# Optimization experiments

Hardware: AMD Instinct MI355X
Metric: run time of the kernel (lower is better)

Reference implementation:

```python
import jax, jax.numpy as jnp
import numpy as np

N = 100000
E = 1600000
D_IN = 128
D_OUT = 128
BN_EPS = 1e-5


def setup_inputs() -> dict:
    key = jax.random.key(0)
    k_x, k_src, k_dst, k_val, k_w = jax.random.split(key, 5)
    x = jax.random.normal(k_x, (N, D_IN), dtype=jnp.float32)
    edge_src = jax.random.randint(k_src, (E,), 0, N, dtype=jnp.int64)
    edge_dst = jax.random.randint(k_dst, (E,), 0, N, dtype=jnp.int64)
    edge_vals = jax.random.uniform(k_val, (E,), dtype=jnp.float32)
    # kaiming-uniform-like init for weight
    bound = float(np.sqrt(6.0 / D_IN))
    weight = jax.random.uniform(k_w, (D_IN, D_OUT), dtype=jnp.float32,
                                minval=-bound, maxval=bound)
    bias = jnp.zeros((D_OUT,), dtype=jnp.float32)
    gamma = jnp.ones((D_OUT,), dtype=jnp.float32)   # BatchNorm weight
    beta = jnp.zeros((D_OUT,), dtype=jnp.float32)   # BatchNorm bias
    return {"x": x, "edge_src": edge_src, "edge_dst": edge_dst,
            "edge_vals": edge_vals, "weight": weight, "bias": bias,
            "gamma": gamma, "beta": beta}


def reference(x, edge_src, edge_dst, edge_vals, weight, bias, gamma, beta):
    # SpMM: out[dst] += val * x[src]  (adj @ x with adj in COO form)
    msgs = x[edge_src] * edge_vals[:, None]            # [E, D_IN]
    agg = jax.ops.segment_sum(msgs, edge_dst, num_segments=N)  # [N, D_IN]
    # Dense linear
    h = jnp.dot(agg, weight) + bias                     # [N, D_OUT]
    # BatchNorm1d (training mode: batch statistics, biased variance)
    mean = jnp.mean(h, axis=0)
    var = jnp.mean(jnp.square(h - mean), axis=0)
    h_norm = (h - mean) * jax.lax.rsqrt(var + BN_EPS)
    return h_norm * gamma + beta
```

## Files before the change

kernel.cpp:

```cpp
#include <hip/hip_runtime.h>
#include <math.h>

#define D 128
#define BSHIFT 9
#define BROWS 512
#define TILE 8192
constexpr float BN_EPS = 1e-5f;
typedef unsigned long long ull;

__device__ __forceinline__ unsigned f2bf_rne(float f) {
    unsigned u = __float_as_uint(f);
    return (u + 0x7FFFu + ((u >> 16) & 1u)) >> 16;
}
__device__ __forceinline__ float bf_lo(unsigned u) { return __uint_as_float(u << 16); }
__device__ __forceinline__ float bf_hi(unsigned u) { return __uint_as_float(u & 0xFFFF0000u); }

__global__ __launch_bounds__(256) void phase1_kernel(
    const float* __restrict__ A,
    const float* __restrict__ W,
    unsigned* __restrict__ yb,
    int n,
    const int* __restrict__ esrc, const int* __restrict__ edst,
    const float* __restrict__ evals,
    uint2* __restrict__ slices,
    int* __restrict__ ofs_t,
    int B, int nwgA, int E)
{
    __shared__ __align__(16) char smem[81920];
    const int tid = threadIdx.x;

    if ((int)blockIdx.x < nwgA) {
        int* h   = (int*)smem;
        int* ps  = h + 256;
        int* cur = ps + 256;
        const int wg = blockIdx.x;
        const int e0 = wg * TILE;
        const int e1 = min(e0 + TILE, E);

        h[tid] = 0;
        __syncthreads();
        for (int e = e0 + tid; e < e1; e += 256)
            atomicAdd(&h[edst[e] >> BSHIFT], 1);
        __syncthreads();

        const int v = h[tid];
        ps[tid] = v;
        __syncthreads();
        for (int off = 1; off < 256; off <<= 1) {
            int t = (tid >= off) ? ps[tid - off] : 0;
            __syncthreads();
            if (tid >= off) ps[tid] += t;
            __syncthreads();
        }
        const int excl = ps[tid] - v;
        if (tid < B) {
            cur[tid] = excl;
            ofs_t[(size_t)tid * nwgA + wg] = excl;
        }
        if (tid == 0) ofs_t[(size_t)B * nwgA + wg] = e1 - e0;
        __syncthreads();

        uint2* slice = slices + (size_t)wg * TILE;
        for (int e = e0 + tid; e < e1; e += 256) {
            int d = edst[e];
            int b = d >> BSHIFT;
            int p = atomicAdd(&cur[b], 1);
            uint2 rec;
            rec.x = (unsigned)(d & (BROWS - 1)) | ((unsigned)esrc[e] << BSHIFT);
            rec.y = __float_as_uint(evals[e]);
            slice[p] = rec;
        }
    } else {
        float* sW = (float*)smem;
        float (*sA)[128] = (float(*)[128])(smem + 65536);

        const float4* W4  = (const float4*)W;
        float4*       sW4 = (float4*)sW;
#pragma unroll
        for (int i = 0; i < 16; i++) sW4[tid + 256 * i] = W4[tid + 256 * i];

        const int row0 = (blockIdx.x - nwgA) * 32;
        const float4* A4  = (const float4*)(A + (size_t)row0 * D);
        float4*       sA4 = (float4*)&sA[0][0];
#pragma unroll
        for (int i = 0; i < 4; i++) {
            int idx = tid + 256 * i;
            sA4[idx] = ((size_t)row0 * D + (size_t)idx * 4 < (size_t)n * D)
                           ? A4[idx] : make_float4(0.f, 0.f, 0.f, 0.f);
        }
        __syncthreads();

        const int tx = tid & 31;
        const int ty = tid >> 5;
        const int c0 = tx * 4;

        float acc[4][4] = {};
        for (int k0 = 0; k0 < 128; k0 += 4) {
            float4 a[4];
#pragma unroll
            for (int j = 0; j < 4; j++)
                a[j] = *(const float4*)&sA[ty + 8 * j][k0];
#pragma unroll
            for (int kk = 0; kk < 4; kk++) {
                const float4 w = *(const float4*)&sW[(k0 + kk) * 128 + c0];
                const float ak[4] = { kk == 0 ? a[0].x : kk == 1 ? a[0].y : kk == 2 ? a[0].z : a[0].w,
                                      kk == 0 ? a[1].x : kk == 1 ? a[1].y : kk == 2 ? a[1].z : a[1].w,
                                      kk == 0 ? a[2].x : kk == 1 ? a[2].y : kk == 2 ? a[2].z : a[2].w,
                                      kk == 0 ? a[3].x : kk == 1 ? a[3].y : kk == 2 ? a[3].z : a[3].w };
#pragma unroll
                for (int j = 0; j < 4; j++) {
                    acc[j][0] += ak[j] * w.x;
                    acc[j][1] += ak[j] * w.y;
                    acc[j][2] += ak[j] * w.z;
                    acc[j][3] += ak[j] * w.w;
                }
            }
        }

#pragma unroll
        for (int j = 0; j < 4; j++) {
            const int row = row0 + ty + 8 * j;
            if (row < n) {
                uint2 o;
                o.x = f2bf_rne(acc[j][0]) | (f2bf_rne(acc[j][1]) << 16);
                o.y = f2bf_rne(acc[j][2]) | (f2bf_rne(acc[j][3]) << 16);
                ((uint2*)(yb + (size_t)row * 64))[tx] = o;
            }
        }
    }
}

__global__ __launch_bounds__(1024) void binB_kernel(
    const uint2* __restrict__ slices,
    const int* __restrict__ ofs_t,
    int* __restrict__ rowptr,
    ull* __restrict__ csr,
    int B, int nwgA, int n)
{
    __shared__ int srow[256];
    __shared__ int erow[256];
    __shared__ int red[256];
    __shared__ int hist[BROWS];
    __shared__ int curs[BROWS];
    __shared__ int ps[BROWS];
    __shared__ int s_bbase;

    const int tid  = threadIdx.x;
    const int b    = blockIdx.x;
    const int w    = tid >> 6;
    const int lane = tid & 63;

    for (int i = tid; i < nwgA; i += 1024) {
        srow[i] = ofs_t[(size_t)b * nwgA + i];
        erow[i] = ofs_t[(size_t)(b + 1) * nwgA + i];
    }
    if (tid < BROWS) hist[tid] = 0;
    __syncthreads();

    if (tid < 256) red[tid] = (tid < nwgA) ? srow[tid] : 0;
    __syncthreads();
    for (int off = 128; off > 0; off >>= 1) {
        if (tid < off) red[tid] += red[tid + off];
        __syncthreads();
    }
    if (tid == 0) s_bbase = red[0];
    __syncthreads();

    for (int wg = w; wg < nwgA; wg += 16) {
        const int s = srow[wg];
        const int e = erow[wg];
        const uint2* run = slices + (size_t)wg * TILE;
        for (int i = s + lane; i < e; i += 64)
            atomicAdd(&hist[run[i].x & (BROWS - 1)], 1);
    }
    __syncthreads();

    int v0 = 0;
    if (tid < BROWS) { v0 = hist[tid]; ps[tid] = v0; }
    __syncthreads();
    for (int off = 1; off < BROWS; off <<= 1) {
        int t = 0;
        if (tid < BROWS && tid >= off) t = ps[tid - off];
        __syncthreads();
        if (tid < BROWS) ps[tid] += t;
        __syncthreads();
    }
    if (tid < BROWS) {
        const int excl = s_bbase + ps[tid] - v0;
        curs[tid] = excl;
        const int r = (b << BSHIFT) + tid;
        if (r < n) rowptr[r] = excl + v0;
    }
    __syncthreads();

    for (int wg = w; wg < nwgA; wg += 16) {
        const int s = srow[wg];
        const int e = erow[wg];
        const uint2* run = slices + (size_t)wg * TILE;
        for (int i = s + lane; i < e; i += 64) {
            uint2 r = run[i];
            int pos = atomicAdd(&curs[r.x & (BROWS - 1)], 1);
            csr[pos] = ((ull)r.y << 32) | (r.x >> BSHIFT);
        }
    }
}

__global__ __launch_bounds__(256) void spmm_stats_kernel(
    const unsigned* __restrict__ yb,
    const int* __restrict__ rowptr,
    const ull* __restrict__ csr,
    float* __restrict__ h,
    float* __restrict__ stats,
    int n)
{
    __shared__ int   rp[65];
    __shared__ float ssum[128];
    __shared__ float ssq[128];

    const int tid       = threadIdx.x;
    const int blockRow0 = blockIdx.x * 64;
    const int wv        = tid >> 6;
    const int lane      = tid & 63;
    const int half      = lane >> 5;
    const int li        = lane & 31;
    const int rbase     = blockRow0 + wv * 16;

    if (tid < 128) { ssum[tid] = 0.f; ssq[tid] = 0.f; }
    if (tid < 65) {
        int idx = blockRow0 + tid - 1;
        rp[tid] = (idx < 0) ? 0 : rowptr[min(idx, n - 1)];
    }
    __syncthreads();

    float s0 = 0.f, s1 = 0.f, s2 = 0.f, s3 = 0.f;
    float q0 = 0.f, q1 = 0.f, q2 = 0.f, q3 = 0.f;

    if (rbase < n) {
        for (int pr = 0; pr < 16; pr += 2) {
            const int  rA    = rbase + pr + half;
            const bool rowOK = rA < n;
            const int  s_    = rowOK ? rp[rA - blockRow0]     : 0;
            const int  e_    = rowOK ? rp[rA - blockRow0 + 1] : 0;
            const int  nA    = e_ - s_;
            const int  nMax  = max(nA, __shfl_xor(nA, 32));

            float a0 = 0.f, a1 = 0.f, a2 = 0.f, a3 = 0.f;
            for (int i = 0; i < nMax; i += 8) {
                ull cd[8];
#pragma unroll
                for (int j = 0; j < 8; j++) {
                    int idx = s_ + i + j;
                    int ce  = (idx < e_) ? idx : (nA ? e_ - 1 : 0);
                    cd[j] = csr[ce];
                }
                uint2 u[8];
                float v[8];
#pragma unroll
                for (int j = 0; j < 8; j++) {
                    u[j] = *(const uint2*)(yb + (size_t)(unsigned)cd[j] * 64 + 2 * li);
                    v[j] = (s_ + i + j < e_)
                               ? __uint_as_float((unsigned)(cd[j] >> 32))
                               : 0.f;
                }
#pragma unroll
                for (int j = 0; j < 8; j++) {
                    a0 += v[j] * bf_lo(u[j].x);
                    a1 += v[j] * bf_hi(u[j].x);
                    a2 += v[j] * bf_lo(u[j].y);
                    a3 += v[j] * bf_hi(u[j].y);
                }
            }

            if (rowOK) {
                *(float4*)&h[(size_t)rA * D + 4 * li] = make_float4(a0, a1, a2, a3);
                s0 += a0; s1 += a1; s2 += a2; s3 += a3;
                q0 += a0 * a0; q1 += a1 * a1; q2 += a2 * a2; q3 += a3 * a3;
            }
        }

        atomicAdd(&ssum[4 * li + 0], s0); atomicAdd(&ssum[4 * li + 1], s1);
        atomicAdd(&ssum[4 * li + 2], s2); atomicAdd(&ssum[4 * li + 3], s3);
        atomicAdd(&ssq [4 * li + 0], q0); atomicAdd(&ssq [4 * li + 1], q1);
        atomicAdd(&ssq [4 * li + 2], q2); atomicAdd(&ssq [4 * li + 3], q3);
    }
    __syncthreads();
    if (tid < 128) {
        atomicAdd(&stats[tid],       ssum[tid]);
        atomicAdd(&stats[128 + tid], ssq[tid]);
    }
}

__global__ __launch_bounds__(256) void bn_apply_kernel(
    float* __restrict__ h,
    const float* __restrict__ stats,
    const float* __restrict__ gamma,
    const float* __restrict__ beta,
    int n)
{
    __shared__ float s_scale[128];
    __shared__ float s_shift[128];
    const int tid = threadIdx.x;
    if (tid < 128) {
        const float invn = 1.0f / (float)n;
        const float mean = stats[tid] * invn;
        const float var  = stats[128 + tid] * invn - mean * mean;
        const float inv  = rsqrtf(var + BN_EPS);
        const float g    = gamma[tid] * inv;
        s_scale[tid] = g;
        s_shift[tid] = beta[tid] - mean * g;
    }
    __syncthreads();

    float4* h4 = (float4*)h;
    const size_t total = (size_t)n * D / 4;
    const size_t stride = (size_t)gridDim.x * blockDim.x;
    for (size_t i = (size_t)blockIdx.x * blockDim.x + tid; i < total; i += stride) {
        float4 v = h4[i];
        const int c = (int)((i * 4) & (D - 1));
        v.x = v.x * s_scale[c]     + s_shift[c];
        v.y = v.y * s_scale[c + 1] + s_shift[c + 1];
        v.z = v.z * s_scale[c + 2] + s_shift[c + 2];
        v.w = v.w * s_scale[c + 3] + s_shift[c + 3];
        h4[i] = v;
    }
}

__global__ __launch_bounds__(256) void spmm_atomic_kernel(
    const float* __restrict__ x,
    const int* __restrict__ esrc, const int* __restrict__ edst,
    const float* __restrict__ eval, float* __restrict__ agg, int E)
{
    int wave  = (blockIdx.x * blockDim.x + threadIdx.x) >> 6;
    int lane  = threadIdx.x & 63;
    int nwave = (gridDim.x * blockDim.x) >> 6;
    for (int e = wave; e < E; e += nwave) {
        int   s = esrc[e];
        int   d = edst[e];
        float v = eval[e];
        const float2 xv = ((const float2*)(x + (size_t)s * D))[lane];
        float* ar = agg + (size_t)d * D + lane * 2;
        atomicAdd(ar,     xv.x * v);
        atomicAdd(ar + 1, xv.y * v);
    }
}

__global__ __launch_bounds__(256) void gemm_stats_kernel(
    const float* __restrict__ A,
    const float* __restrict__ W,
    float* __restrict__ h,
    float* __restrict__ stats,
    int n)
{
    __shared__ float sW[128 * 128];
    __shared__ float sA[32][128];
    const int tid = threadIdx.x;
    const float4* W4  = (const float4*)W;
    float4*       sW4 = (float4*)sW;
#pragma unroll
    for (int i = 0; i < 16; i++) sW4[tid + 256 * i] = W4[tid + 256 * i];
    const int row0 = blockIdx.x * 32;
    const float4* A4  = (const float4*)(A + (size_t)row0 * D);
    float4*       sA4 = (float4*)&sA[0][0];
#pragma unroll
    for (int i = 0; i < 4; i++) {
        int idx = tid + 256 * i;
        sA4[idx] = ((size_t)row0 * D + (size_t)idx * 4 < (size_t)n * D)
                       ? A4[idx] : make_float4(0.f, 0.f, 0.f, 0.f);
    }
    __syncthreads();
    const int tx = tid & 31, ty = tid >> 5, c0 = tx * 4;
    float acc[4][4] = {};
    for (int k = 0; k < 128; k++) {
        const float4 w = *(const float4*)&sW[k * 128 + c0];
#pragma unroll
        for (int j = 0; j < 4; j++) {
            const float a = sA[ty + 8 * j][k];
            acc[j][0] += a * w.x; acc[j][1] += a * w.y;
            acc[j][2] += a * w.z; acc[j][3] += a * w.w;
        }
    }
#pragma unroll
    for (int j = 0; j < 4; j++) {
        const int row = row0 + ty + 8 * j;
        if (row < n)
            *(float4*)&h[(size_t)row * D + c0] =
                make_float4(acc[j][0], acc[j][1], acc[j][2], acc[j][3]);
    }
    __syncthreads();
    float* csum = &sA[0][0];
    float* csq  = csum + 128;
    if (tid < 128) { csum[tid] = 0.f; csq[tid] = 0.f; }
    __syncthreads();
#pragma unroll
    for (int c = 0; c < 4; c++) {
        float s = 0.f, q = 0.f;
#pragma unroll
        for (int j = 0; j < 4; j++) { s += acc[j][c]; q += acc[j][c] * acc[j][c]; }
        atomicAdd(&csum[c0 + c], s);
        atomicAdd(&csq[c0 + c], q);
    }
    __syncthreads();
    if (tid < 128) {
        atomicAdd(&stats[tid],       csum[tid]);
        atomicAdd(&stats[128 + tid], csq[tid]);
    }
}

extern "C" void kernel_launch(void* const* d_in, const int* in_sizes, int n_in,
                              void* d_out, int out_size, void* d_ws, size_t ws_size,
                              hipStream_t stream)
{
    const float* x     = (const float*)d_in[0];
    const int*   esrc  = (const int*)d_in[1];
    const int*   edst  = (const int*)d_in[2];
    const float* evals = (const float*)d_in[3];
    const float* W     = (const float*)d_in[4];
    const float* gamma = (const float*)d_in[6];
    const float* beta  = (const float*)d_in[7];
    float* out = (float*)d_out;

    const int n = in_sizes[0] / D;
    const int E = in_sizes[1];

    const int B     = (n + BROWS - 1) >> BSHIFT;
    const int nwgA  = (E + TILE - 1) / TILE;
    const int ngemm = (n + 31) / 32;

    unsigned* yb     = (unsigned*)d_ws;
    float*    stats  = (float*)(yb + (size_t)n * 64);
    int*      ofs_t  = (int*)(stats + 256);
    int*      rowptr = ofs_t + (size_t)(B + 1) * nwgA;
    size_t    w_off  = (size_t)n * 64 + 256 + (size_t)(B + 1) * nwgA + n;
    w_off += (w_off & 1);
    uint2*    slices = (uint2*)((unsigned*)d_ws + w_off);
    ull*      csr    = (ull*)(slices + (size_t)nwgA * TILE);
    const size_t need = (w_off + (size_t)nwgA * TILE * 2 + (size_t)E * 2) * 4;

    if (ws_size >= need && B <= 256 && nwgA <= 256) {
        hipMemsetAsync(stats, 0, 256 * 4, stream);
        phase1_kernel<<<nwgA + ngemm, 256, 0, stream>>>(
            x, W, yb, n, esrc, edst, evals, slices, ofs_t, B, nwgA, E);
        binB_kernel<<<B, 1024, 0, stream>>>(
            slices, ofs_t, rowptr, csr, B, nwgA, n);
        spmm_stats_kernel<<<(n + 63) / 64, 256, 0, stream>>>(
            yb, rowptr, csr, out, stats, n);
        bn_apply_kernel<<<2048, 256, 0, stream>>>(out, stats, gamma, beta, n);
    } else {
        float* agg = (float*)d_ws;
        float* st  = agg + (size_t)n * D;
        hipMemsetAsync(d_ws, 0, ((size_t)n * D + 256) * 4, stream);
        spmm_atomic_kernel<<<4096, 256, 0, stream>>>(x, esrc, edst, evals, agg, E);
        gemm_stats_kernel<<<(n + 31) / 32, 256, 0, stream>>>(agg, W, out, st, n);
        bn_apply_kernel<<<2048, 256, 0, stream>>>(out, st, gamma, beta, n);
    }
}
```

Baseline: 309.0 us.

## Read GEMM weights from global memory and gather 16-byte rows in SpMM

The GEMM branch of phase1 no longer stages the 64KB weight matrix in LDS. It reads weight float4s straight from global memory (cached in L1/L2), which cuts LDS per block from 80KB to 16KB so more blocks can be resident. The SpMM kernel now assigns four rows per wavefront, with 16 lanes each loading 16 bytes (8 bf16 features) per neighbour, and unrolls by 4 edges. The trade-off is more per-row LDS atomics for the statistics, smaller per-row edge batches, and weight reads that depend on cache hit rates.

```diff
diff --git a/kernel.cpp b/kernel.cpp
--- a/kernel.cpp
+++ b/kernel.cpp
@@ -26,7 +26,7 @@
     int* __restrict__ ofs_t,
     int B, int nwgA, int E)
 {
-    __shared__ __align__(16) char smem[81920];
+    __shared__ __align__(16) char smem[16384];
     const int tid = threadIdx.x;
 
     if ((int)blockIdx.x < nwgA) {
@@ -71,13 +71,7 @@
             slice[p] = rec;
         }
     } else {
-        float* sW = (float*)smem;
-        float (*sA)[128] = (float(*)[128])(smem + 65536);
-
-        const float4* W4  = (const float4*)W;
-        float4*       sW4 = (float4*)sW;
-#pragma unroll
-        for (int i = 0; i < 16; i++) sW4[tid + 256 * i] = W4[tid + 256 * i];
+        float (*sA)[128] = (float(*)[128])smem;
 
         const int row0 = (blockIdx.x - nwgA) * 32;
         const float4* A4  = (const float4*)(A + (size_t)row0 * D);
@@ -93,6 +87,7 @@
         const int tx = tid & 31;
         const int ty = tid >> 5;
         const int c0 = tx * 4;
+        const float4* W4 = (const float4*)W;
 
         float acc[4][4] = {};
         for (int k0 = 0; k0 < 128; k0 += 4) {
@@ -102,7 +97,7 @@
                 a[j] = *(const float4*)&sA[ty + 8 * j][k0];
 #pragma unroll
             for (int kk = 0; kk < 4; kk++) {
-                const float4 w = *(const float4*)&sW[(k0 + kk) * 128 + c0];
+                const float4 w = W4[(k0 + kk) * 32 + tx];
                 const float ak[4] = { kk == 0 ? a[0].x : kk == 1 ? a[0].y : kk == 2 ? a[0].z : a[0].w,
                                       kk == 0 ? a[1].x : kk == 1 ? a[1].y : kk == 2 ? a[1].z : a[1].w,
                                       kk == 0 ? a[2].x : kk == 1 ? a[2].y : kk == 2 ? a[2].z : a[2].w,
@@ -221,8 +216,8 @@
     const int blockRow0 = blockIdx.x * 64;
     const int wv        = tid >> 6;
     const int lane      = tid & 63;
-    const int half      = lane >> 5;
-    const int li        = lane & 31;
+    const int qw        = lane >> 4;
+    const int li4       = lane & 15;
     const int rbase     = blockRow0 + wv * 16;
 
     if (tid < 128) { ssum[tid] = 0.f; ssq[tid] = 0.f; }
@@ -232,56 +227,59 @@
     }
     __syncthreads();
 
-    float s0 = 0.f, s1 = 0.f, s2 = 0.f, s3 = 0.f;
-    float q0 = 0.f, q1 = 0.f, q2 = 0.f, q3 = 0.f;
-
     if (rbase < n) {
-        for (int pr = 0; pr < 16; pr += 2) {
-            const int  rA    = rbase + pr + half;
-            const bool rowOK = rA < n;
-            const int  s_    = rowOK ? rp[rA - blockRow0]     : 0;
-            const int  e_    = rowOK ? rp[rA - blockRow0 + 1] : 0;
+        for (int q = 0; q < 4; ++q) {
+            const int  r     = rbase + 4 * q + qw;
+            const bool rowOK = r < n;
+            const int  s_    = rowOK ? rp[r - blockRow0]     : 0;
+            const int  e_    = rowOK ? rp[r - blockRow0 + 1] : 0;
             const int  nA    = e_ - s_;
-            const int  nMax  = max(nA, __shfl_xor(nA, 32));
+            int m = max(nA, __shfl_xor(nA, 16));
+            m = max(m, __shfl_xor(m, 32));
 
             float a0 = 0.f, a1 = 0.f, a2 = 0.f, a3 = 0.f;
-            for (int i = 0; i < nMax; i += 8) {
-                ull cd[8];
-#pragma unroll
-                for (int j = 0; j < 8; j++) {
-                    int idx = s_ + i + j;
-                    int ce  = (idx < e_) ? idx : (nA ? e_ - 1 : 0);
-                    cd[j] = csr[ce];
-                }
-                uint2 u[8];
-                float v[8];
-#pragma unroll
-                for (int j = 0; j < 8; j++) {
-                    u[j] = *(const uint2*)(yb + (size_t)(unsigned)cd[j] * 64 + 2 * li);
-                    v[j] = (s_ + i + j < e_)
-                               ? __uint_as_float((unsigned)(cd[j] >> 32))
-                               : 0.f;
-                }
-#pragma unroll
-                for (int j = 0; j < 8; j++) {
-                    a0 += v[j] * bf_lo(u[j].x);
-                    a1 += v[j] * bf_hi(u[j].x);
-                    a2 += v[j] * bf_lo(u[j].y);
-                    a3 += v[j] * bf_hi(u[j].y);
-                }
+            float a4 = 0.f, a5 = 0.f, a6 = 0.f, a7 = 0.f;
+
+            for (int i = 0; i < m; i += 4) {
+                int i0 = s_ + i;
+                ull c0 = csr[(i0 + 0 < e_) ? i0 + 0 : (nA ? e_ - 1 : 0)];
+                ull c1 = csr[(i0 + 1 < e_) ? i0 + 1 : (nA ? e_ - 1 : 0)];
+                ull c2 = csr[(i0 + 2 < e_) ? i0 + 2 : (nA ? e_ - 1 : 0)];
+                ull c3 = csr[(i0 + 3 < e_) ? i0 + 3 : (nA ? e_ - 1 : 0)];
+
+                uint4 u0 = *(const uint4*)(yb + (size_t)(unsigned)c0 * 64 + 4 * li4);
+                uint4 u1 = *(const uint4*)(yb + (size_t)(unsigned)c1 * 64 + 4 * li4);
+                uint4 u2 = *(const uint4*)(yb + (size_t)(unsigned)c2 * 64 + 4 * li4);
+                uint4 u3 = *(const uint4*)(yb + (size_t)(unsigned)c3 * 64 + 4 * li4);
+
+                float v0 = (i0 + 0 < e_) ? __uint_as_float((unsigned)(c0 >> 32)) : 0.f;
+                float v1 = (i0 + 1 < e_) ? __uint_as_float((unsigned)(c1 >> 32)) : 0.f;
+                float v2 = (i0 + 2 < e_) ? __uint_as_float((unsigned)(c2 >> 32)) : 0.f;
+                float v3 = (i0 + 3 < e_) ? __uint_as_float((unsigned)(c3 >> 32)) : 0.f;
+
+                a0 += v0 * bf_lo(u0.x) + v1 * bf_lo(u1.x) + v2 * bf_lo(u2.x) + v3 * bf_lo(u3.x);
+                a1 += v0 * bf_hi(u0.x) + v1 * bf_hi(u1.x) + v2 * bf_hi(u2.x) + v3 * bf_hi(u3.x);
+                a2 += v0 * bf_lo(u0.y) + v1 * bf_lo(u1.y) + v2 * bf_lo(u2.y) + v3 * bf_lo(u3.y);
+                a3 += v0 * bf_hi(u0.y) + v1 * bf_hi(u1.y) + v2 * bf_hi(u2.y) + v3 * bf_hi(u3.y);
+                a4 += v0 * bf_lo(u0.z) + v1 * bf_lo(u1.z) + v2 * bf_lo(u2.z) + v3 * bf_lo(u3.z);
+                a5 += v0 * bf_hi(u0.z) + v1 * bf_hi(u1.z) + v2 * bf_hi(u2.z) + v3 * bf_hi(u3.z);
+                a6 += v0 * bf_lo(u0.w) + v1 * bf_lo(u1.w) + v2 * bf_lo(u2.w) + v3 * bf_lo(u3.w);
+                a7 += v0 * bf_hi(u0.w) + v1 * bf_hi(u1.w) + v2 * bf_hi(u2.w) + v3 * bf_hi(u3.w);
             }
 
             if (rowOK) {
-                *(float4*)&h[(size_t)rA * D + 4 * li] = make_float4(a0, a1, a2, a3);
-                s0 += a0; s1 += a1; s2 += a2; s3 += a3;
-                q0 += a0 * a0; q1 += a1 * a1; q2 += a2 * a2; q3 += a3 * a3;
+                *(float4*)&h[(size_t)r * D + 8 * li4]     = make_float4(a0, a1, a2, a3);
+                *(float4*)&h[(size_t)r * D + 8 * li4 + 4] = make_float4(a4, a5, a6, a7);
+                atomicAdd(&ssum[8 * li4 + 0], a0); atomicAdd(&ssum[8 * li4 + 1], a1);
+                atomicAdd(&ssum[8 * li4 + 2], a2); atomicAdd(&ssum[8 * li4 + 3], a3);
+                atomicAdd(&ssum[8 * li4 + 4], a4); atomicAdd(&ssum[8 * li4 + 5], a5);
+                atomicAdd(&ssum[8 * li4 + 6], a6); atomicAdd(&ssum[8 * li4 + 7], a7);
+                atomicAdd(&ssq[8 * li4 + 0], a0 * a0); atomicAdd(&ssq[8 * li4 + 1], a1 * a1);
+                atomicAdd(&ssq[8 * li4 + 2], a2 * a2); atomicAdd(&ssq[8 * li4 + 3], a3 * a3);
+                atomicAdd(&ssq[8 * li4 + 4], a4 * a4); atomicAdd(&ssq[8 * li4 + 5], a5 * a5);
+                atomicAdd(&ssq[8 * li4 + 6], a6 * a6); atomicAdd(&ssq[8 * li4 + 7], a7 * a7);
             }
         }
-
-        atomicAdd(&ssum[4 * li + 0], s0); atomicAdd(&ssum[4 * li + 1], s1);
-        atomicAdd(&ssum[4 * li + 2], s2); atomicAdd(&ssum[4 * li + 3], s3);
-        atomicAdd(&ssq [4 * li + 0], q0); atomicAdd(&ssq [4 * li + 1], q1);
-        atomicAdd(&ssq [4 * li + 2], q2); atomicAdd(&ssq [4 * li + 3], q3);
     }
     __syncthreads();
     if (tid < 128) {
```

New measurement: 382.3 us. 1.24x slower.

## Count per-row degrees with global atomics and drop W from shared memory

Applied to the files above, without the earlier changes.

The binning pass now counts edges per destination row with global atomics into a zeroed rowcnt array, so binB_kernel no longer re-reads all slices to build its per-row histogram. The GEMM path reads W directly from global/L2 instead of staging 64KB in LDS, which cuts the shared allocation from 80KB to 16KB and should raise occupancy for both phase1 roles. The cost is 1.6M global atomics on a 100K-entry array, an extra memset, and W loads that now go through the cache on every k step rather than coming from LDS.

```diff
diff --git a/kernel.cpp b/kernel.cpp
--- a/kernel.cpp
+++ b/kernel.cpp
@@ -24,9 +24,10 @@
     const float* __restrict__ evals,
     uint2* __restrict__ slices,
     int* __restrict__ ofs_t,
+    int* __restrict__ rowcnt,
     int B, int nwgA, int E)
 {
-    __shared__ __align__(16) char smem[81920];
+    __shared__ __align__(16) char smem[16384];
     const int tid = threadIdx.x;
 
     if ((int)blockIdx.x < nwgA) {
@@ -65,19 +66,14 @@
             int d = edst[e];
             int b = d >> BSHIFT;
             int p = atomicAdd(&cur[b], 1);
+            atomicAdd(&rowcnt[d], 1);
             uint2 rec;
             rec.x = (unsigned)(d & (BROWS - 1)) | ((unsigned)esrc[e] << BSHIFT);
             rec.y = __float_as_uint(evals[e]);
             slice[p] = rec;
         }
     } else {
-        float* sW = (float*)smem;
-        float (*sA)[128] = (float(*)[128])(smem + 65536);
-
-        const float4* W4  = (const float4*)W;
-        float4*       sW4 = (float4*)sW;
-#pragma unroll
-        for (int i = 0; i < 16; i++) sW4[tid + 256 * i] = W4[tid + 256 * i];
+        float (*sA)[128] = (float(*)[128])smem;
 
         const int row0 = (blockIdx.x - nwgA) * 32;
         const float4* A4  = (const float4*)(A + (size_t)row0 * D);
@@ -92,7 +88,7 @@
 
         const int tx = tid & 31;
         const int ty = tid >> 5;
-        const int c0 = tx * 4;
+        const float4* W4 = (const float4*)W;
 
         float acc[4][4] = {};
         for (int k0 = 0; k0 < 128; k0 += 4) {
@@ -102,7 +98,7 @@
                 a[j] = *(const float4*)&sA[ty + 8 * j][k0];
 #pragma unroll
             for (int kk = 0; kk < 4; kk++) {
-                const float4 w = *(const float4*)&sW[(k0 + kk) * 128 + c0];
+                const float4 w = W4[(k0 + kk) * 32 + tx];
                 const float ak[4] = { kk == 0 ? a[0].x : kk == 1 ? a[0].y : kk == 2 ? a[0].z : a[0].w,
                                       kk == 0 ? a[1].x : kk == 1 ? a[1].y : kk == 2 ? a[1].z : a[1].w,
                                       kk == 0 ? a[2].x : kk == 1 ? a[2].y : kk == 2 ? a[2].z : a[2].w,
@@ -133,6 +129,7 @@
 __global__ __launch_bounds__(1024) void binB_kernel(
     const uint2* __restrict__ slices,
     const int* __restrict__ ofs_t,
+    const int* __restrict__ rowcnt,
     int* __restrict__ rowptr,
     ull* __restrict__ csr,
     int B, int nwgA, int n)
@@ -140,7 +137,6 @@
     __shared__ int srow[256];
     __shared__ int erow[256];
     __shared__ int red[256];
-    __shared__ int hist[BROWS];
     __shared__ int curs[BROWS];
     __shared__ int ps[BROWS];
     __shared__ int s_bbase;
@@ -154,7 +150,6 @@
         srow[i] = ofs_t[(size_t)b * nwgA + i];
         erow[i] = ofs_t[(size_t)(b + 1) * nwgA + i];
     }
-    if (tid < BROWS) hist[tid] = 0;
     __syncthreads();
 
     if (tid < 256) red[tid] = (tid < nwgA) ? srow[tid] : 0;
@@ -166,17 +161,12 @@
     if (tid == 0) s_bbase = red[0];
     __syncthreads();
 
-    for (int wg = w; wg < nwgA; wg += 16) {
-        const int s = srow[wg];
-        const int e = erow[wg];
-        const uint2* run = slices + (size_t)wg * TILE;
-        for (int i = s + lane; i < e; i += 64)
-            atomicAdd(&hist[run[i].x & (BROWS - 1)], 1);
-    }
-    __syncthreads();
-
     int v0 = 0;
-    if (tid < BROWS) { v0 = hist[tid]; ps[tid] = v0; }
+    if (tid < BROWS) {
+        const int r = (b << BSHIFT) + tid;
+        v0 = (r < n) ? rowcnt[r] : 0;
+        ps[tid] = v0;
+    }
     __syncthreads();
     for (int off = 1; off < BROWS; off <<= 1) {
         int t = 0;
@@ -430,7 +420,8 @@
     float*    stats  = (float*)(yb + (size_t)n * 64);
     int*      ofs_t  = (int*)(stats + 256);
     int*      rowptr = ofs_t + (size_t)(B + 1) * nwgA;
-    size_t    w_off  = (size_t)n * 64 + 256 + (size_t)(B + 1) * nwgA + n;
+    int*      rowcnt = rowptr + n;
+    size_t    w_off  = (size_t)n * 64 + 256 + (size_t)(B + 1) * nwgA + 2 * (size_t)n;
     w_off += (w_off & 1);
     uint2*    slices = (uint2*)((unsigned*)d_ws + w_off);
     ull*      csr    = (ull*)(slices + (size_t)nwgA * TILE);
@@ -438,10 +429,11 @@
 
     if (ws_size >= need && B <= 256 && nwgA <= 256) {
         hipMemsetAsync(stats, 0, 256 * 4, stream);
+        hipMemsetAsync(rowcnt, 0, (size_t)n * 4, stream);
         phase1_kernel<<<nwgA + ngemm, 256, 0, stream>>>(
-            x, W, yb, n, esrc, edst, evals, slices, ofs_t, B, nwgA, E);
+            x, W, yb, n, esrc, edst, evals, slices, ofs_t, rowcnt, B, nwgA, E);
         binB_kernel<<<B, 1024, 0, stream>>>(
-            slices, ofs_t, rowptr, csr, B, nwgA, n);
+            slices, ofs_t, rowcnt, rowptr, csr, B, nwgA, n);
         spmm_stats_kernel<<<(n + 63) / 64, 256, 0, stream>>>(
             yb, rowptr, csr, out, stats, n);
         bn_apply_kernel<<<2048, 256, 0, stream>>>(out, stats, gamma, beta, n);
```

Result: slower. 339.1 us (+9.7%).

## Compute dense X·W projection with split-bf16 MFMA instead of scalar FP32 FMAs

Applied to the files above, without the earlier changes.

Replaces the FP32 scalar-FMA GEMM in phase1 with MFMA 16x16x32 bf16 instructions, using a three-term hi/lo bf16 split of both X and W to keep near-FP32 accuracy. A new small kernel pre-splits and transposes W into bf16 hi/lo arrays, which the GEMM blocks read directly from global memory instead of staging the full FP32 W in LDS. GEMM tiles grow to 64 rows, and LDS use drops from 80 KB to about 34 KB, which should allow more resident workgroups, shared with the edge-binning blocks. In exchange it adds an extra kernel launch, an LDS round-trip for the output epilogue, and some precision loss from the 3-product split.

```diff
diff --git a/kernel.cpp b/kernel.cpp
--- a/kernel.cpp
+++ b/kernel.cpp
@@ -7,6 +7,8 @@
 #define TILE 8192
 constexpr float BN_EPS = 1e-5f;
 typedef unsigned long long ull;
+typedef __attribute__((ext_vector_type(8))) short short8v;
+typedef __attribute__((ext_vector_type(4))) float f32x4;
 
 __device__ __forceinline__ unsigned f2bf_rne(float f) {
     unsigned u = __float_as_uint(f);
@@ -14,10 +16,30 @@
 }
 __device__ __forceinline__ float bf_lo(unsigned u) { return __uint_as_float(u << 16); }
 __device__ __forceinline__ float bf_hi(unsigned u) { return __uint_as_float(u & 0xFFFF0000u); }
+__device__ __forceinline__ void split_bf16(float f, unsigned& hi, unsigned& lo) {
+    hi = f2bf_rne(f);
+    lo = f2bf_rne(f - bf_lo(hi));
+}
+
+__global__ __launch_bounds__(256) void wprep_kernel(
+    const float* __restrict__ W,
+    unsigned short* __restrict__ whiT,
+    unsigned short* __restrict__ wloT)
+{
+    int idx = blockIdx.x * 256 + threadIdx.x;
+    if (idx < 128 * 128) {
+        int k = idx >> 7, nn = idx & 127;
+        unsigned hi, lo;
+        split_bf16(W[idx], hi, lo);
+        whiT[nn * 128 + k] = (unsigned short)hi;
+        wloT[nn * 128 + k] = (unsigned short)lo;
+    }
+}
 
 __global__ __launch_bounds__(256) void phase1_kernel(
     const float* __restrict__ A,
-    const float* __restrict__ W,
+    const unsigned short* __restrict__ whiT,
+    const unsigned short* __restrict__ wloT,
     unsigned* __restrict__ yb,
     int n,
     const int* __restrict__ esrc, const int* __restrict__ edst,
@@ -26,7 +48,7 @@
     int* __restrict__ ofs_t,
     int B, int nwgA, int E)
 {
-    __shared__ __align__(16) char smem[81920];
+    __shared__ __align__(16) char smem[34816];
     const int tid = threadIdx.x;
 
     if ((int)blockIdx.x < nwgA) {
@@ -71,61 +93,95 @@
             slice[p] = rec;
         }
     } else {
-        float* sW = (float*)smem;
-        float (*sA)[128] = (float(*)[128])(smem + 65536);
-
-        const float4* W4  = (const float4*)W;
-        float4*       sW4 = (float4*)sW;
-#pragma unroll
-        for (int i = 0; i < 16; i++) sW4[tid + 256 * i] = W4[tid + 256 * i];
-
-        const int row0 = (blockIdx.x - nwgA) * 32;
-        const float4* A4  = (const float4*)(A + (size_t)row0 * D);
-        float4*       sA4 = (float4*)&sA[0][0];
-#pragma unroll
-        for (int i = 0; i < 4; i++) {
-            int idx = tid + 256 * i;
-            sA4[idx] = ((size_t)row0 * D + (size_t)idx * 4 < (size_t)n * D)
-                           ? A4[idx] : make_float4(0.f, 0.f, 0.f, 0.f);
-        }
-        __syncthreads();
-
-        const int tx = tid & 31;
-        const int ty = tid >> 5;
-        const int c0 = tx * 4;
-
-        float acc[4][4] = {};
-        for (int k0 = 0; k0 < 128; k0 += 4) {
-            float4 a[4];
-#pragma unroll
-            for (int j = 0; j < 4; j++)
-                a[j] = *(const float4*)&sA[ty + 8 * j][k0];
-#pragma unroll
-            for (int kk = 0; kk < 4; kk++) {
-                const float4 w = *(const float4*)&sW[(k0 + kk) * 128 + c0];
-                const float ak[4] = { kk == 0 ? a[0].x : kk == 1 ? a[0].y : kk == 2 ? a[0].z : a[0].w,
-                                      kk == 0 ? a[1].x : kk == 1 ? a[1].y : kk == 2 ? a[1].z : a[1].w,
-                                      kk == 0 ? a[2].x : kk == 1 ? a[2].y : kk == 2 ? a[2].z : a[2].w,
-                                      kk == 0 ? a[3].x : kk == 1 ? a[3].y : kk == 2 ? a[3].z : a[3].w };
-#pragma unroll
-                for (int j = 0; j < 4; j++) {
-                    acc[j][0] += ak[j] * w.x;
-                    acc[j][1] += ak[j] * w.y;
-                    acc[j][2] += ak[j] * w.z;
-                    acc[j][3] += ak[j] * w.w;
+        unsigned short* xh = (unsigned short*)smem;
+        unsigned short* xl = xh + 64 * 136;
+
+        const int row0 = ((int)blockIdx.x - nwgA) * 64;
+        const float4* A4 = (const float4*)(A + (size_t)row0 * D);
+
+#pragma unroll
+        for (int i = 0; i < 8; i++) {
+            const int idx = tid + 256 * i;
+            const int row = idx >> 5, c4 = idx & 31;
+            float4 v = (row0 + row < n) ? A4[idx]
+                                        : make_float4(0.f, 0.f, 0.f, 0.f);
+            unsigned h0, h1, h2, h3, l0, l1, l2, l3;
+            split_bf16(v.x, h0, l0); split_bf16(v.y, h1, l1);
+            split_bf16(v.z, h2, l2); split_bf16(v.w, h3, l3);
+            unsigned short* ph = xh + (size_t)row * 136 + c4 * 4;
+            unsigned short* pl = xl + (size_t)row * 136 + c4 * 4;
+            *(uint2*)ph = make_uint2(h0 | (h1 << 16), h2 | (h3 << 16));
+            *(uint2*)pl = make_uint2(l0 | (l1 << 16), l2 | (l3 << 16));
+        }
+        __syncthreads();
+
+        const int wv = tid >> 6;
+        const int l  = tid & 63;
+        const int lr = l & 15;
+        const int lg = l >> 4;
+        const int colbase = wv * 32;
+
+        f32x4 acc[4][2];
+#pragma unroll
+        for (int rt = 0; rt < 4; rt++)
+#pragma unroll
+            for (int ct = 0; ct < 2; ct++)
+                acc[rt][ct] = (f32x4){0.f, 0.f, 0.f, 0.f};
+
+        for (int k0 = 0; k0 < 128; k0 += 32) {
+            const int kf = k0 + lg * 8;
+            short8v ah[4], al[4];
+#pragma unroll
+            for (int rt = 0; rt < 4; rt++) {
+                const unsigned short* p = xh + (size_t)(16 * rt + lr) * 136 + kf;
+                const unsigned short* q = xl + (size_t)(16 * rt + lr) * 136 + kf;
+                ah[rt] = *(const short8v*)p;
+                al[rt] = *(const short8v*)q;
+            }
+            short8v bh[2], bl[2];
+#pragma unroll
+            for (int ct = 0; ct < 2; ct++) {
+                const int nidx = colbase + 16 * ct + lr;
+                bh[ct] = *(const short8v*)(whiT + (size_t)nidx * 128 + kf);
+                bl[ct] = *(const short8v*)(wloT + (size_t)nidx * 128 + kf);
+            }
+#pragma unroll
+            for (int rt = 0; rt < 4; rt++)
+#pragma unroll
+                for (int ct = 0; ct < 2; ct++) {
+                    acc[rt][ct] = __builtin_amdgcn_mfma_f32_16x16x32_bf16(
+                        ah[rt], bh[ct], acc[rt][ct], 0, 0, 0);
+                    acc[rt][ct] = __builtin_amdgcn_mfma_f32_16x16x32_bf16(
+                        ah[rt], bl[ct], acc[rt][ct], 0, 0, 0);
+                    acc[rt][ct] = __builtin_amdgcn_mfma_f32_16x16x32_bf16(
+                        al[rt], bh[ct], acc[rt][ct], 0, 0, 0);
                 }
-            }
-        }
-
-#pragma unroll
-        for (int j = 0; j < 4; j++) {
-            const int row = row0 + ty + 8 * j;
-            if (row < n) {
-                uint2 o;
-                o.x = f2bf_rne(acc[j][0]) | (f2bf_rne(acc[j][1]) << 16);
-                o.y = f2bf_rne(acc[j][2]) | (f2bf_rne(acc[j][3]) << 16);
-                ((uint2*)(yb + (size_t)row * 64))[tx] = o;
-            }
+        }
+        __syncthreads();
+
+        float* Cl = (float*)smem;
+#pragma unroll
+        for (int rt = 0; rt < 4; rt++)
+#pragma unroll
+            for (int ct = 0; ct < 2; ct++)
+#pragma unroll
+                for (int r = 0; r < 4; r++) {
+                    const int row = 16 * rt + lg * 4 + r;
+                    const int col = colbase + 16 * ct + lr;
+                    Cl[row * 132 + col] = acc[rt][ct][r];
+                }
+        __syncthreads();
+
+#pragma unroll
+        for (int i = 0; i < 8; i++) {
+            const int idx = tid + 256 * i;
+            const int row = idx >> 5, p = idx & 31;
+            const float* c4 = Cl + row * 132 + p * 4;
+            uint2 o;
+            o.x = f2bf_rne(c4[0]) | (f2bf_rne(c4[1]) << 16);
+            o.y = f2bf_rne(c4[2]) | (f2bf_rne(c4[3]) << 16);
+            if (row0 + row < n)
+                ((uint2*)(yb + (size_t)(row0 + row) * 64))[p] = o;
         }
     }
 }
@@ -424,22 +480,26 @@
 
     const int B     = (n + BROWS - 1) >> BSHIFT;
     const int nwgA  = (E + TILE - 1) / TILE;
-    const int ngemm = (n + 31) / 32;
-
-    unsigned* yb     = (unsigned*)d_ws;
-    float*    stats  = (float*)(yb + (size_t)n * 64);
-    int*      ofs_t  = (int*)(stats + 256);
-    int*      rowptr = ofs_t + (size_t)(B + 1) * nwgA;
-    size_t    w_off  = (size_t)n * 64 + 256 + (size_t)(B + 1) * nwgA + n;
+    const int ngemm = (n + 63) / 64;
+
+    unsigned*       yb     = (unsigned*)d_ws;
+    float*          stats  = (float*)(yb + (size_t)n * 64);
+    unsigned short* whiT   = (unsigned short*)(stats + 256);
+    unsigned short* wloT   = whiT + 16384;
+    int*            ofs_t  = (int*)(wloT + 16384);
+    int*            rowptr = ofs_t + (size_t)(B + 1) * nwgA;
+    size_t w_off = (size_t)n * 64 + 256 + 16384
+                 + (size_t)(B + 1) * nwgA + n;
     w_off += (w_off & 1);
-    uint2*    slices = (uint2*)((unsigned*)d_ws + w_off);
-    ull*      csr    = (ull*)(slices + (size_t)nwgA * TILE);
+    uint2* slices = (uint2*)((unsigned*)d_ws + w_off);
+    ull*   csr    = (ull*)(slices + (size_t)nwgA * TILE);
     const size_t need = (w_off + (size_t)nwgA * TILE * 2 + (size_t)E * 2) * 4;
 
     if (ws_size >= need && B <= 256 && nwgA <= 256) {
         hipMemsetAsync(stats, 0, 256 * 4, stream);
+        wprep_kernel<<<64, 256, 0, stream>>>(W, whiT, wloT);
         phase1_kernel<<<nwgA + ngemm, 256, 0, stream>>>(
-            x, W, yb, n, esrc, edst, evals, slices, ofs_t, B, nwgA, E);
+            x, whiT, wloT, yb, n, esrc, edst, evals, slices, ofs_t, B, nwgA, E);
         binB_kernel<<<B, 1024, 0, stream>>>(
             slices, ofs_t, rowptr, csr, B, nwgA, n);
         spmm_stats_kernel<<<(n + 63) / 64, 256, 0, stream>>>(
```

New measurement: 291.6 us. 5.6% less time.
